# Kernel optimization log

Measured on AMD Instinct MI355X. Metric: run time of the kernel, lower is better.

The kernel has to match this reference:

```python
import jax, jax.numpy as jnp
import numpy as np

B, T, C = 4, 128, 512
NH, HS = 8, 64          # n_head, head_dim = C // NH
ORDER = 3               # attention_order
SCALE = 1.0 / np.sqrt(HS)


def setup_inputs() -> dict:
    key = jax.random.key(0)
    ks = jax.random.split(key, 7)
    s = 0.02
    return {
        "x": jax.random.normal(ks[0], (B, T, C), jnp.float32),
        "Wp0": jax.random.normal(ks[1], (C, C), jnp.float32) * s,
        "Wp1": jax.random.normal(ks[2], (C, C), jnp.float32) * s,
        "Wp2": jax.random.normal(ks[3], (C, C), jnp.float32) * s,
        "Wv0": jax.random.normal(ks[4], (HS, HS), jnp.float32) * s,
        "Wv1": jax.random.normal(ks[5], (HS, HS), jnp.float32) * s,
        "Wc": jax.random.normal(ks[6], (C, C), jnp.float32) * s,
    }


def _heads(x, W):
    # Linear then split heads: (B,T,C) -> (B,NH,T,HS)
    return (x @ W).reshape(B, T, NH, HS).transpose(0, 2, 1, 3)


def _causal_mask(t, order):
    # indices grid [T]^order, True where i0 >= i1 >= ... >= i_{order-1}
    idx = jnp.arange(t)
    g = jnp.stack(jnp.meshgrid(*([idx] * order), indexing='ij'), axis=-1)
    return jnp.all(jnp.diff(g, axis=-1) <= 0, axis=-1)


def reference(x, Wp0, Wp1, Wp2, Wv0, Wv1, Wc):
    p0 = _heads(x, Wp0)  # (B,NH,T,HS)
    p1 = _heads(x, Wp1)
    p2 = _heads(x, Wp2)

    # pairwise scores, then higher-order broadcast exactly as the torch einsum
    # ('bh...i,bhkd->bh...ik' sums the key over d and broadcasts — faithful).
    att = jnp.einsum('bhid,bhjd->bhij', p0, p1) * SCALE        # (B,NH,T,T)
    att = jnp.einsum('bh...i,bhkd->bh...ik', att, p2)          # (B,NH,T,T,T)

    mask = _causal_mask(T, ORDER)[None, None]                  # (1,1,T,T,T)
    att = jnp.where(mask, att, -jnp.inf)
    att = jax.nn.softmax(att.reshape(B, NH, T, T * T), axis=-1)

    # value tensors with broadcasted elementwise product over the order dims
    V0 = (p1 @ Wv0)[:, :, :, None, :]   # (B,NH,T,1,HS)
    V1 = (p2 @ Wv1)[:, :, None, :, :]   # (B,NH,1,T,HS)
    V = (V0 * V1).reshape(B, NH, T * T, HS)

    y = jnp.einsum('bhij,bhjd->bhid', att, V)                  # (B,NH,T,HS)
    y = y.transpose(0, 2, 1, 3).reshape(B, T, C)
    return y @ Wc
```

## Files before the change

### kernel.cpp

```cpp
#include <hip/hip_runtime.h>
#include <hip/hip_bf16.h>
#include <math.h>

#define B 4
#define T 128
#define C 512
#define NH 8
#define HS 64
#define BH (B*NH)

typedef __attribute__((ext_vector_type(8))) short bf16x8;
typedef __attribute__((ext_vector_type(4))) float f32x4;

__device__ __forceinline__ unsigned short bfc(float x) {
    return __builtin_bit_cast(unsigned short, __float2bfloat16(x));
}
__device__ __forceinline__ unsigned int pk_bf16(float a, float b) {
    return (unsigned int)bfc(a) | ((unsigned int)bfc(b) << 16);
}
__device__ __forceinline__ float lo_f(unsigned int g) {
    return __builtin_bit_cast(float, g << 16);
}
__device__ __forceinline__ float hi_f(unsigned int g) {
    return __builtin_bit_cast(float, g & 0xffff0000u);
}

__global__ __launch_bounds__(256) void proj_kernel(
    const float* __restrict__ X,
    const float* __restrict__ Wp0, const float* __restrict__ Wp1, const float* __restrict__ Wp2,
    unsigned short* __restrict__ p0b, unsigned short* __restrict__ p1b,
    unsigned short* __restrict__ p2b, float* __restrict__ rr)
{
    __shared__ __align__(16) unsigned short As[64][72];
    __shared__ __align__(16) unsigned short Bs[64][72];
    __shared__ float Ls[64][69];
    __shared__ float sRS[4][64];
    const int z = blockIdx.z;
    const float* W = (z == 0) ? Wp0 : (z == 1) ? Wp1 : Wp2;
    const int m0 = blockIdx.y * 64, n0 = blockIdx.x * 64;
    const int tid = threadIdx.x;
    const int w = tid >> 6, lane = tid & 63, quad = lane >> 4, l16 = lane & 15;
    f32x4 acc[4];
    #pragma unroll
    for (int mt = 0; mt < 4; ++mt) acc[mt] = (f32x4){0.f, 0.f, 0.f, 0.f};

    for (int k0 = 0; k0 < 512; k0 += 64) {
        __syncthreads();
        #pragma unroll
        for (int it = 0; it < 2; ++it) {
            const int q = tid + it * 256;
            const int row = q >> 3, c8 = (q & 7) * 8;
            const float4 a = *(const float4*)&X[(size_t)(m0 + row) * 512 + k0 + c8];
            const float4 b = *(const float4*)&X[(size_t)(m0 + row) * 512 + k0 + c8 + 4];
            uint4 o;
            o.x = pk_bf16(a.x, a.y);
            o.y = pk_bf16(a.z, a.w);
            o.z = pk_bf16(b.x, b.y);
            o.w = pk_bf16(b.z, b.w);
            *(uint4*)&As[row][c8] = o;
        }
        #pragma unroll
        for (int it = 0; it < 4; ++it) {
            const int q = tid + it * 256;
            const int row = q >> 4, c4 = (q & 15) * 4;
            const float4 v = *(const float4*)&W[(size_t)(k0 + row) * 512 + n0 + c4];
            Ls[row][c4 + 0] = v.x; Ls[row][c4 + 1] = v.y;
            Ls[row][c4 + 2] = v.z; Ls[row][c4 + 3] = v.w;
        }
        __syncthreads();
        #pragma unroll
        for (int it = 0; it < 2; ++it) {
            const int q = tid + it * 256;
            const int nrow = q >> 3, k8 = (q & 7) * 8;
            uint4 o;
            o.x = pk_bf16(Ls[k8 + 0][nrow], Ls[k8 + 1][nrow]);
            o.y = pk_bf16(Ls[k8 + 2][nrow], Ls[k8 + 3][nrow]);
            o.z = pk_bf16(Ls[k8 + 4][nrow], Ls[k8 + 5][nrow]);
            o.w = pk_bf16(Ls[k8 + 6][nrow], Ls[k8 + 7][nrow]);
            *(uint4*)&Bs[nrow][k8] = o;
        }
        __syncthreads();
        #pragma unroll
        for (int kt = 0; kt < 2; ++kt) {
            const bf16x8 b8 = *(const bf16x8*)&Bs[w * 16 + l16][kt * 32 + quad * 8];
            #pragma unroll
            for (int mt = 0; mt < 4; ++mt) {
                const bf16x8 a8 = *(const bf16x8*)&As[mt * 16 + l16][kt * 32 + quad * 8];
                acc[mt] = __builtin_amdgcn_mfma_f32_16x16x32_bf16(a8, b8, acc[mt], 0, 0, 0);
            }
        }
    }

    {
        const int n = n0 + w * 16 + l16;
        const int h = n >> 6, d = n & 63;
        unsigned short* pz = (z == 0) ? p0b : (z == 1) ? p1b : p2b;
        #pragma unroll
        for (int mt = 0; mt < 4; ++mt) {
            #pragma unroll
            for (int r = 0; r < 4; ++r) {
                const int m = m0 + mt * 16 + quad * 4 + r;
                const int bb = m >> 7, t = m & 127;
                pz[((size_t)(bb * NH + h) * T + t) * HS + d] = bfc(acc[mt][r]);
            }
        }
    }
    if (z == 2) {
        #pragma unroll
        for (int mt = 0; mt < 4; ++mt)
            #pragma unroll
            for (int r = 0; r < 4; ++r) {
                float v = acc[mt][r];
                v += __shfl_xor(v, 1, 64); v += __shfl_xor(v, 2, 64);
                v += __shfl_xor(v, 4, 64); v += __shfl_xor(v, 8, 64);
                if (l16 == 0) sRS[w][mt * 16 + quad * 4 + r] = v;
            }
        __syncthreads();
        if (tid < 64) {
            const float s = sRS[0][tid] + sRS[1][tid] + sRS[2][tid] + sRS[3][tid];
            const int m = m0 + tid, bb = m >> 7, tl = m & 127, h = n0 >> 6;
            rr[(bb * NH + h) * T + tl] = s;
        }
    }
}

__global__ __launch_bounds__(256) void attn_kernel(
    const unsigned short* __restrict__ p0b, const unsigned short* __restrict__ p1b,
    const unsigned short* __restrict__ p2b, const float* __restrict__ rr,
    const float* __restrict__ Wv0, const float* __restrict__ Wv1,
    unsigned short* __restrict__ Yb)
{
    __shared__ __align__(16) union {
        struct {
            unsigned short sWv[64][72];
            unsigned short sVst[64][136];
        } v;
        unsigned short sE[128 * 128];
    } u;
    __shared__ float sS[4][128];
    __shared__ float srr[128];
    __shared__ float sZ[4];

    const int bid = blockIdx.x;
    const int bh = bid & (BH - 1);
    const int ig = bid >> 5;
    const int tid = threadIdx.x;
    const int w = tid >> 6;
    const int lane = tid & 63;
    const int quad = lane >> 4;
    const int l16 = lane & 15;

    if (tid < 128) srr[tid] = rr[bh * T + tid];

    #pragma unroll
    for (int it = 0; it < 4; ++it) {
        const int k = (tid >> 4) + it * 16;
        const int d0 = (tid & 15) * 4;
        const float4 wv = *(const float4*)&Wv0[(size_t)k * 64 + d0];
        u.v.sWv[d0 + 0][k] = bfc(wv.x); u.v.sWv[d0 + 1][k] = bfc(wv.y);
        u.v.sWv[d0 + 2][k] = bfc(wv.z); u.v.sWv[d0 + 3][k] = bfc(wv.w);
    }
    __syncthreads();

    #pragma unroll
    for (int nn = 0; nn < 2; ++nn) {
        const int nt = w + nn * 4;
        f32x4 vacc[4];
        #pragma unroll
        for (int mt = 0; mt < 4; ++mt) vacc[mt] = (f32x4){0.f, 0.f, 0.f, 0.f};
        #pragma unroll
        for (int kt = 0; kt < 2; ++kt) {
            const bf16x8 b8 = *(const bf16x8*)&p1b[((size_t)bh * T + nt * 16 + l16) * HS + kt * 32 + quad * 8];
            #pragma unroll
            for (int mt = 0; mt < 4; ++mt) {
                const bf16x8 a8 = *(const bf16x8*)&u.v.sWv[mt * 16 + l16][kt * 32 + quad * 8];
                vacc[mt] = __builtin_amdgcn_mfma_f32_16x16x32_bf16(a8, b8, vacc[mt], 0, 0, 0);
            }
        }
        #pragma unroll
        for (int mt = 0; mt < 4; ++mt)
            #pragma unroll
            for (int r = 0; r < 4; ++r)
                u.v.sVst[mt * 16 + quad * 4 + r][nt * 16 + l16] = bfc(vacc[mt][r]);
    }
    __syncthreads();

    uint2 v0r[8];
    #pragma unroll
    for (int mt = 0; mt < 8; ++mt)
        v0r[mt] = *(const uint2*)&u.v.sVst[(w << 4) + l16][(mt << 4) + (quad << 2)];
    #pragma unroll
    for (int it = 0; it < 4; ++it) {
        const int k = (tid >> 4) + it * 16;
        const int d0 = (tid & 15) * 4;
        const float4 wv = *(const float4*)&Wv1[(size_t)k * 64 + d0];
        u.v.sWv[d0 + 0][k] = bfc(wv.x); u.v.sWv[d0 + 1][k] = bfc(wv.y);
        u.v.sWv[d0 + 2][k] = bfc(wv.z); u.v.sWv[d0 + 3][k] = bfc(wv.w);
    }
    __syncthreads();

    #pragma unroll
    for (int nn = 0; nn < 2; ++nn) {
        const int nt = w + nn * 4;
        f32x4 vacc[4];
        #pragma unroll
        for (int mt = 0; mt < 4; ++mt) vacc[mt] = (f32x4){0.f, 0.f, 0.f, 0.f};
        #pragma unroll
        for (int kt = 0; kt < 2; ++kt) {
            const bf16x8 b8 = *(const bf16x8*)&p2b[((size_t)bh * T + nt * 16 + l16) * HS + kt * 32 + quad * 8];
            #pragma unroll
            for (int mt = 0; mt < 4; ++mt) {
                const bf16x8 a8 = *(const bf16x8*)&u.v.sWv[mt * 16 + l16][kt * 32 + quad * 8];
                vacc[mt] = __builtin_amdgcn_mfma_f32_16x16x32_bf16(a8, b8, vacc[mt], 0, 0, 0);
            }
        }
        #pragma unroll
        for (int mt = 0; mt < 4; ++mt)
            #pragma unroll
            for (int r = 0; r < 4; ++r)
                u.v.sVst[mt * 16 + quad * 4 + r][nt * 16 + l16] = bfc(vacc[mt][r]);
    }
    __syncthreads();

    uint4 v1r[4];
    #pragma unroll
    for (int kt = 0; kt < 4; ++kt)
        v1r[kt] = *(const uint4*)&u.v.sVst[(w << 4) + l16][(quad << 3) + (kt << 5)];

    {
        const int qr = l16 & 3;
        const int irow = (qr & 1) ? (32 * qr + 31 - ig) : (32 * qr + ig);
        const unsigned short* ap = p0b + ((size_t)bh * T + irow) * HS + (quad << 3);
        const unsigned short* bp = p1b + (size_t)bh * T * HS + (quad << 3);
        f32x4 s0 = (f32x4){0.f, 0.f, 0.f, 0.f};
        f32x4 s1 = (f32x4){0.f, 0.f, 0.f, 0.f};
        #pragma unroll
        for (int kt = 0; kt < 2; ++kt) {
            const bf16x8 a8 = *(const bf16x8*)(ap + (kt << 5));
            const bf16x8 b0 = *(const bf16x8*)(bp + (size_t)((w << 5) + l16) * HS + (kt << 5));
            const bf16x8 b1 = *(const bf16x8*)(bp + (size_t)((w << 5) + 16 + l16) * HS + (kt << 5));
            s0 = __builtin_amdgcn_mfma_f32_16x16x32_bf16(a8, b0, s0, 0, 0, 0);
            s1 = __builtin_amdgcn_mfma_f32_16x16x32_bf16(a8, b1, s1, 0, 0, 0);
        }
        if (quad == 0) {
            #pragma unroll
            for (int r = 0; r < 4; ++r) {
                sS[r][(w << 5) + l16]      = s0[r] * 0.125f;
                sS[r][(w << 5) + 16 + l16] = s1[r] * 0.125f;
            }
        }
    }
    __syncthreads();

    const float L2E = 1.4426950408889634f;

    for (int qq = 3; qq >= 0; --qq) {
        const int i = (qq & 1) ? (32 * qq + 31 - ig) : (32 * qq + ig);
        const float* sSq = sS[qq];

        float mhat;
        {
            float a0 = (lane <= i) ? fabsf(sSq[lane]) : 0.f;
            float a1 = (64 + lane <= i) ? fabsf(sSq[64 + lane]) : 0.f;
            float r0 = (lane <= i) ? fabsf(srr[lane]) : 0.f;
            float r1 = (64 + lane <= i) ? fabsf(srr[64 + lane]) : 0.f;
            float aS = fmaxf(a0, a1), aR = fmaxf(r0, r1);
            #pragma unroll
            for (int off = 32; off; off >>= 1) {
                aS = fmaxf(aS, __shfl_xor(aS, off, 64));
                aR = fmaxf(aR, __shfl_xor(aR, off, 64));
            }
            mhat = aS * aR;
        }

        const float bexp = -mhat * L2E;
        const int mtmax = i >> 4;
        const int cc = tid & 15;
        const int rowin = tid >> 4;
        const int k0l = cc << 3;
        float zacc = 0.f;

        float rk[8];
        *(float4*)&rk[0] = *(const float4*)&srr[k0l];
        *(float4*)&rk[4] = *(const float4*)&srr[k0l + 4];
        const int npass = mtmax + 1;
        for (int p = 0; p < npass; ++p) {
            const int jj = (p << 4) + rowin;
            uint4 o = {0u, 0u, 0u, 0u};
            if (jj <= i && k0l <= jj) {
                const float aL = sSq[jj] * L2E;
                const int dlim = jj - k0l;
                float e[8];
                #pragma unroll
                for (int q = 0; q < 8; ++q) {
                    const float ex = __builtin_amdgcn_exp2f(fmaf(aL, rk[q], bexp));
                    e[q] = (q <= dlim) ? ex : 0.f;
                    zacc += e[q];
                }
                o.x = pk_bf16(e[0], e[1]);
                o.y = pk_bf16(e[2], e[3]);
                o.z = pk_bf16(e[4], e[5]);
                o.w = pk_bf16(e[6], e[7]);
            }
            *(uint4*)&u.sE[(jj << 7) + ((cc ^ (jj & 7)) << 3)] = o;
        }
        #pragma unroll
        for (int off = 32; off; off >>= 1) zacc += __shfl_xor(zacc, off, 64);
        if (lane == 0) sZ[w] = zacc;
        __syncthreads();

        f32x4 acc[8];
        #pragma unroll
        for (int mt = 0; mt < 8; ++mt) acc[mt] = (f32x4){0.f, 0.f, 0.f, 0.f};
        #pragma unroll
        for (int mt = 0; mt < 8; ++mt) {
            if (mt <= mtmax) {
                #pragma unroll
                for (int kt = 0; kt < 4; ++kt) {
                    if (kt <= (mt >> 1)) {
                        const int ch = ((kt << 2) + quad) ^ (l16 & 7);
                        const bf16x8 a8 = *(const bf16x8*)&u.sE[(((mt << 4) + l16) << 7) + (ch << 3)];
                        acc[mt] = __builtin_amdgcn_mfma_f32_16x16x32_bf16(
                            a8, __builtin_bit_cast(bf16x8, v1r[kt]), acc[mt], 0, 0, 0);
                    }
                }
            }
        }
        const float Z = sZ[0] + sZ[1] + sZ[2] + sZ[3];

        float part = 0.f;
        #pragma unroll
        for (int mt = 0; mt < 8; ++mt) {
            if (mt < mtmax) {
                const uint2 uu = v0r[mt];
                part = fmaf(lo_f(uu.x), acc[mt][0], part);
                part = fmaf(hi_f(uu.x), acc[mt][1], part);
                part = fmaf(lo_f(uu.y), acc[mt][2], part);
                part = fmaf(hi_f(uu.y), acc[mt][3], part);
            } else if (mt == mtmax) {
                const uint2 uu = v0r[mt];
                const int jb = (mt << 4) + (quad << 2);
                if (jb + 0 <= i) part = fmaf(lo_f(uu.x), acc[mt][0], part);
                if (jb + 1 <= i) part = fmaf(hi_f(uu.x), acc[mt][1], part);
                if (jb + 2 <= i) part = fmaf(lo_f(uu.y), acc[mt][2], part);
                if (jb + 3 <= i) part = fmaf(hi_f(uu.y), acc[mt][3], part);
            }
        }
        part += __shfl_xor(part, 16, 64);
        part += __shfl_xor(part, 32, 64);
        if (lane < 16) {
            const int bb = bh >> 3, hh = bh & 7;
            Yb[((size_t)(bb * T + i) * C) + hh * HS + (w << 4) + l16] = bfc(part / Z);
        }
        __syncthreads();
    }
}

__global__ __launch_bounds__(256) void outmm_kernel(
    const unsigned short* __restrict__ Ab, const float* __restrict__ Wc,
    float* __restrict__ OUT)
{
    __shared__ __align__(16) unsigned short As[64][72];
    __shared__ __align__(16) unsigned short Bs[64][72];
    __shared__ float Ls[64][69];
    const int m0 = blockIdx.y * 64, n0 = blockIdx.x * 64;
    const int tid = threadIdx.x;
    const int w = tid >> 6, lane = tid & 63, quad = lane >> 4, l16 = lane & 15;
    f32x4 acc[4];
    #pragma unroll
    for (int mt = 0; mt < 4; ++mt) acc[mt] = (f32x4){0.f, 0.f, 0.f, 0.f};
    for (int k0 = 0; k0 < 512; k0 += 64) {
        __syncthreads();
        #pragma unroll
        for (int it = 0; it < 2; ++it) {
            const int q = tid + it * 256;
            const int row = q >> 3, c8 = (q & 7) * 8;
            *(uint4*)&As[row][c8] = *(const uint4*)&Ab[(size_t)(m0 + row) * 512 + k0 + c8];
        }
        #pragma unroll
        for (int it = 0; it < 4; ++it) {
            const int q = tid + it * 256;
            const int row = q >> 4, c4 = (q & 15) * 4;
            const float4 v = *(const float4*)&Wc[(size_t)(k0 + row) * 512 + n0 + c4];
            Ls[row][c4 + 0] = v.x; Ls[row][c4 + 1] = v.y;
            Ls[row][c4 + 2] = v.z; Ls[row][c4 + 3] = v.w;
        }
        __syncthreads();
        #pragma unroll
        for (int it = 0; it < 2; ++it) {
            const int q = tid + it * 256;
            const int nrow = q >> 3, k8 = (q & 7) * 8;
            uint4 o;
            o.x = pk_bf16(Ls[k8 + 0][nrow], Ls[k8 + 1][nrow]);
            o.y = pk_bf16(Ls[k8 + 2][nrow], Ls[k8 + 3][nrow]);
            o.z = pk_bf16(Ls[k8 + 4][nrow], Ls[k8 + 5][nrow]);
            o.w = pk_bf16(Ls[k8 + 6][nrow], Ls[k8 + 7][nrow]);
            *(uint4*)&Bs[nrow][k8] = o;
        }
        __syncthreads();
        #pragma unroll
        for (int kt = 0; kt < 2; ++kt) {
            const bf16x8 b8 = *(const bf16x8*)&Bs[w * 16 + l16][kt * 32 + quad * 8];
            #pragma unroll
            for (int mt = 0; mt < 4; ++mt) {
                const bf16x8 a8 = *(const bf16x8*)&As[mt * 16 + l16][kt * 32 + quad * 8];
                acc[mt] = __builtin_amdgcn_mfma_f32_16x16x32_bf16(a8, b8, acc[mt], 0, 0, 0);
            }
        }
    }
    const int n = n0 + w * 16 + l16;
    #pragma unroll
    for (int mt = 0; mt < 4; ++mt)
        #pragma unroll
        for (int r = 0; r < 4; ++r) {
            const int mrow = m0 + mt * 16 + quad * 4 + r;
            OUT[(size_t)mrow * 512 + n] = acc[mt][r];
        }
}

extern "C" void kernel_launch(void* const* d_in, const int* in_sizes, int n_in,
                              void* d_out, int out_size, void* d_ws, size_t ws_size,
                              hipStream_t stream)
{
    const float* x   = (const float*)d_in[0];
    const float* Wp0 = (const float*)d_in[1];
    const float* Wp1 = (const float*)d_in[2];
    const float* Wp2 = (const float*)d_in[3];
    const float* Wv0 = (const float*)d_in[4];
    const float* Wv1 = (const float*)d_in[5];
    const float* Wc  = (const float*)d_in[6];
    float* out = (float*)d_out;

    char* w8 = (char*)d_ws;
    const size_t HB = 512 * 1024;
    unsigned short* p0b = (unsigned short*)(w8 + 0 * HB);
    unsigned short* p1b = (unsigned short*)(w8 + 1 * HB);
    unsigned short* p2b = (unsigned short*)(w8 + 2 * HB);
    unsigned short* Yb  = (unsigned short*)(w8 + 3 * HB);
    float*          rr  = (float*)        (w8 + 4 * HB);

    proj_kernel <<<dim3(8, 8, 3), 256, 0, stream>>>(x, Wp0, Wp1, Wp2, p0b, p1b, p2b, rr);
    attn_kernel <<<dim3(1024), 256, 0, stream>>>(p0b, p1b, p2b, rr, Wv0, Wv1, Yb);
    outmm_kernel<<<dim3(8, 8), 256, 0, stream>>>(Yb, Wc, out);
}
```

Before: 125.4 us.

## Process eight query rows per block with double-buffered score tile

Each attention block now handles eight query rows instead of four, so the grid is halved and the per-block setup (Wv staging, V1 projection, srr load) is amortised over more rows. The exp tile in shared memory is double-buffered so the trailing barrier at the end of each row iteration can be dropped. The max-based stabiliser is computed once per block from all eight rows rather than per row with causal masking. This doubles shared memory for the tile, which may reduce occupancy, and a looser shared stabiliser risks underflow for rows whose scores are much smaller than the block maximum.

```diff
diff --git a/kernel.cpp b/kernel.cpp
--- a/kernel.cpp
+++ b/kernel.cpp
@@ -135,11 +135,11 @@
             unsigned short sWv[64][72];
             unsigned short sVst[64][136];
         } v;
-        unsigned short sE[128 * 128];
+        unsigned short sE[2][128 * 128];
     } u;
-    __shared__ float sS[4][128];
+    __shared__ float sS[8][128];
     __shared__ float srr[128];
-    __shared__ float sZ[4];
+    __shared__ float sZ[2][4];
 
     const int bid = blockIdx.x;
     const int bh = bid & (BH - 1);
@@ -226,10 +226,9 @@
     #pragma unroll
     for (int kt = 0; kt < 4; ++kt)
         v1r[kt] = *(const uint4*)&u.v.sVst[(w << 4) + l16][(quad << 3) + (kt << 5)];
-
     {
-        const int qr = l16 & 3;
-        const int irow = (qr & 1) ? (32 * qr + 31 - ig) : (32 * qr + ig);
+        const int qr = l16 & 7;
+        const int irow = (qr & 1) ? (16 * qr + 15 - ig) : (16 * qr + ig);
         const unsigned short* ap = p0b + ((size_t)bh * T + irow) * HS + (quad << 3);
         const unsigned short* bp = p1b + (size_t)bh * T * HS + (quad << 3);
         f32x4 s0 = (f32x4){0.f, 0.f, 0.f, 0.f};
@@ -242,11 +241,11 @@
             s0 = __builtin_amdgcn_mfma_f32_16x16x32_bf16(a8, b0, s0, 0, 0, 0);
             s1 = __builtin_amdgcn_mfma_f32_16x16x32_bf16(a8, b1, s1, 0, 0, 0);
         }
-        if (quad == 0) {
+        if (quad < 2) {
             #pragma unroll
             for (int r = 0; r < 4; ++r) {
-                sS[r][(w << 5) + l16]      = s0[r] * 0.125f;
-                sS[r][(w << 5) + 16 + l16] = s1[r] * 0.125f;
+                sS[quad * 4 + r][(w << 5) + l16]      = s0[r] * 0.125f;
+                sS[quad * 4 + r][(w << 5) + 16 + l16] = s1[r] * 0.125f;
             }
         }
     }
@@ -254,35 +253,37 @@
 
     const float L2E = 1.4426950408889634f;
 
-    for (int qq = 3; qq >= 0; --qq) {
-        const int i = (qq & 1) ? (32 * qq + 31 - ig) : (32 * qq + ig);
+    float mhat;
+    {
+        float aS = 0.f;
+        #pragma unroll
+        for (int q = 0; q < 8; ++q) {
+            aS = fmaxf(aS, fabsf(sS[q][lane]));
+            aS = fmaxf(aS, fabsf(sS[q][64 + lane]));
+        }
+        float aR = fmaxf(fabsf(srr[lane]), fabsf(srr[64 + lane]));
+        #pragma unroll
+        for (int off = 32; off; off >>= 1) {
+            aS = fmaxf(aS, __shfl_xor(aS, off, 64));
+            aR = fmaxf(aR, __shfl_xor(aR, off, 64));
+        }
+        mhat = aS * aR;
+    }
+    const float bexp = -mhat * L2E;
+    const int cc = tid & 15;
+    const int rowin = tid >> 4;
+    const int k0l = cc << 3;
+    float rk[8];
+    *(float4*)&rk[0] = *(const float4*)&srr[k0l];
+    *(float4*)&rk[4] = *(const float4*)&srr[k0l + 4];
+
+    for (int qq = 7; qq >= 0; --qq) {
+        const int i = (qq & 1) ? (16 * qq + 15 - ig) : (16 * qq + ig);
         const float* sSq = sS[qq];
-
-        float mhat;
-        {
-            float a0 = (lane <= i) ? fabsf(sSq[lane]) : 0.f;
-            float a1 = (64 + lane <= i) ? fabsf(sSq[64 + lane]) : 0.f;
-            float r0 = (lane <= i) ? fabsf(srr[lane]) : 0.f;
-            float r1 = (64 + lane <= i) ? fabsf(srr[64 + lane]) : 0.f;
-            float aS = fmaxf(a0, a1), aR = fmaxf(r0, r1);
-            #pragma unroll
-            for (int off = 32; off; off >>= 1) {
-                aS = fmaxf(aS, __shfl_xor(aS, off, 64));
-                aR = fmaxf(aR, __shfl_xor(aR, off, 64));
-            }
-            mhat = aS * aR;
-        }
-
-        const float bexp = -mhat * L2E;
         const int mtmax = i >> 4;
-        const int cc = tid & 15;
-        const int rowin = tid >> 4;
-        const int k0l = cc << 3;
+        const int buf = qq & 1;
         float zacc = 0.f;
 
-        float rk[8];
-        *(float4*)&rk[0] = *(const float4*)&srr[k0l];
-        *(float4*)&rk[4] = *(const float4*)&srr[k0l + 4];
         const int npass = mtmax + 1;
         for (int p = 0; p < npass; ++p) {
             const int jj = (p << 4) + rowin;
@@ -302,11 +303,11 @@
                 o.z = pk_bf16(e[4], e[5]);
                 o.w = pk_bf16(e[6], e[7]);
             }
-            *(uint4*)&u.sE[(jj << 7) + ((cc ^ (jj & 7)) << 3)] = o;
+            *(uint4*)&u.sE[buf][(jj << 7) + ((cc ^ (jj & 7)) << 3)] = o;
         }
         #pragma unroll
         for (int off = 32; off; off >>= 1) zacc += __shfl_xor(zacc, off, 64);
-        if (lane == 0) sZ[w] = zacc;
+        if (lane == 0) sZ[buf][w] = zacc;
         __syncthreads();
 
         f32x4 acc[8];
@@ -319,14 +320,14 @@
                 for (int kt = 0; kt < 4; ++kt) {
                     if (kt <= (mt >> 1)) {
                         const int ch = ((kt << 2) + quad) ^ (l16 & 7);
-                        const bf16x8 a8 = *(const bf16x8*)&u.sE[(((mt << 4) + l16) << 7) + (ch << 3)];
+                        const bf16x8 a8 = *(const bf16x8*)&u.sE[buf][(((mt << 4) + l16) << 7) + (ch << 3)];
                         acc[mt] = __builtin_amdgcn_mfma_f32_16x16x32_bf16(
                             a8, __builtin_bit_cast(bf16x8, v1r[kt]), acc[mt], 0, 0, 0);
                     }
                 }
             }
         }
-        const float Z = sZ[0] + sZ[1] + sZ[2] + sZ[3];
+        const float Z = sZ[buf][0] + sZ[buf][1] + sZ[buf][2] + sZ[buf][3];
 
         float part = 0.f;
         #pragma unroll
@@ -352,7 +353,6 @@
             const int bb = bh >> 3, hh = bh & 7;
             Yb[((size_t)(bb * T + i) * C) + hh * HS + (w << 4) + l16] = bfc(part / Z);
         }
-        __syncthreads();
     }
 }
 
@@ -440,6 +440,6 @@
     float*          rr  = (float*)        (w8 + 4 * HB);
 
     proj_kernel <<<dim3(8, 8, 3), 256, 0, stream>>>(x, Wp0, Wp1, Wp2, p0b, p1b, p2b, rr);
-    attn_kernel <<<dim3(1024), 256, 0, stream>>>(p0b, p1b, p2b, rr, Wv0, Wv1, Yb);
+    attn_kernel <<<dim3(512), 256, 0, stream>>>(p0b, p1b, p2b, rr, Wv0, Wv1, Yb);
     outmm_kernel<<<dim3(8, 8), 256, 0, stream>>>(Yb, Wc, out);
 }
```

Result: faster. 118.0 us (-5.9%).
